# Kernel tuning notes

Measured on AMD Instinct MI355X. Metric: run time of the kernel, lower is better.

## Reference

```python
import jax, jax.numpy as jnp
import numpy as np

N = 100000   # nodes
E = 1600000  # edges (avg degree 16)
D = 128      # input = hidden = out dim
L = 4        # num_layers
EPS = 1e-5   # LayerNorm eps


def setup_inputs() -> dict:
    key = jax.random.key(0)
    k0, k1, k2, k3, k4 = jax.random.split(key, 5)
    in_feat = jax.random.normal(k0, (N, D), dtype=jnp.float32)
    edge_index = jax.random.randint(k1, (2, E), 0, N, dtype=jnp.int32)
    s = 1.0 / np.sqrt(D)
    # GraphConv params per layer: lin_rel (weight+bias), lin_root (weight, no bias)
    W_rel = jax.random.uniform(k2, (L, D, D), jnp.float32, -s, s)
    b_rel = jax.random.uniform(k3, (L, D), jnp.float32, -s, s)
    W_root = jax.random.uniform(k4, (L, D, D), jnp.float32, -s, s)
    # single shared LayerNorm module in the torch code
    ln_gamma = jnp.ones((D,), jnp.float32)
    ln_beta = jnp.zeros((D,), jnp.float32)
    return {"in_feat": in_feat, "edge_index": edge_index, "W_rel": W_rel,
            "b_rel": b_rel, "W_root": W_root, "ln_gamma": ln_gamma, "ln_beta": ln_beta}


def _layer_norm(h, gamma, beta):
    mu = jnp.mean(h, axis=-1, keepdims=True)
    var = jnp.mean(jnp.square(h - mu), axis=-1, keepdims=True)
    return (h - mu) * jax.lax.rsqrt(var + EPS) * gamma + beta


def _graph_conv(h, W_r, b_r, W_rt, src, dst):
    # PyG GraphConv: out_i = lin_rel(sum_{j->i} x_j) + lin_root(x_i)
    agg = jax.ops.segment_sum(h[src], dst, num_segments=N)  # [N, D]
    return agg @ W_r + b_r + h @ W_rt


def reference(in_feat, edge_index, W_rel, b_rel, W_root, ln_gamma, ln_beta):
    src, dst = edge_index[0], edge_index[1]
    # input layer: conv -> ReLU -> LayerNorm -> dropout(p=0)
    h = _graph_conv(in_feat, W_rel[0], b_rel[0], W_root[0], src, dst)
    h = _layer_norm(jax.nn.relu(h), ln_gamma, ln_beta)
    # middle layers with residual
    for l in range(1, L - 1):
        nh = _graph_conv(h, W_rel[l], b_rel[l], W_root[l], src, dst)
        h = _layer_norm(jax.nn.relu(nh + h), ln_gamma, ln_beta)
    # output layer: conv only
    return _graph_conv(h, W_rel[L - 1], b_rel[L - 1], W_root[L - 1], src, dst)
```

## Files before the change

kernel.cpp:

```cpp
#include <hip/hip_runtime.h>
#include <cstddef>

#define N_NODES 100000
#define N_PAD   100032
#define N_EDGES 1600000
#define DIM 128
#define LN_EPS 1e-5f
#define ZROW   N_NODES
#define COL_CAP 3200000

#define B_SHIFT 9
#define B_SIZE  512
#define N_BKT   196
#define EPB     4096
#define NBLK    ((N_EDGES + EPB - 1) / EPB)

typedef short bf16x8 __attribute__((ext_vector_type(8)));
typedef float f32x4 __attribute__((ext_vector_type(4)));
typedef float f32x2 __attribute__((ext_vector_type(2)));

__device__ __forceinline__ float asf(uint u) {
    union { uint i; float f; } c; c.i = u; return c.f;
}
__device__ __forceinline__ float bf2f(uint u) { return asf(u << 16); }
__device__ __forceinline__ ushort f2bf(float x) {
    union { float f; uint i; } c; c.f = x;
    uint r = c.i + 0x7fffu + ((c.i >> 16) & 1u);
    return (ushort)(r >> 16);
}

__device__ __forceinline__ void accp(f32x2* acc, uint p) {
    f32x2 v;
    v.x = asf(p << 16);
    v.y = asf(p & 0xffff0000u);
    *acc += v;
}
__device__ __forceinline__ void accq(f32x2* a, uint4 p) {
    accp(&a[0], p.x); accp(&a[1], p.y); accp(&a[2], p.z); accp(&a[3], p.w);
}


__global__ __launch_bounds__(256) void bhist_kernel(const int* __restrict__ dst,
                                                    int* __restrict__ bcount) {
    __shared__ int lh[N_BKT];
    const int tid = threadIdx.x;
    if (tid < N_BKT) lh[tid] = 0;
    __syncthreads();
    const int base = blockIdx.x * EPB;
    #pragma unroll
    for (int k = 0; k < 16; ++k) {
        int t = base + tid + k * 256;
        if (t < N_EDGES) atomicAdd(&lh[dst[t] >> B_SHIFT], 1);
    }
    __syncthreads();
    if (tid < N_BKT && lh[tid]) atomicAdd(&bcount[tid], lh[tid]);
}

__global__ __launch_bounds__(256) void bscan_kernel(const int* __restrict__ bcount,
                                                    int* __restrict__ bstart,
                                                    int* __restrict__ gcur) {
    __shared__ int s[256];
    const int tid = threadIdx.x;
    int v = (tid < N_BKT) ? bcount[tid] : 0;
    s[tid] = v;
    __syncthreads();
    for (int off = 1; off < 256; off <<= 1) {
        int t = (tid >= off) ? s[tid - off] : 0;
        __syncthreads();
        s[tid] += t;
        __syncthreads();
    }
    if (tid < N_BKT) { int e = s[tid] - v; bstart[tid] = e; gcur[tid] = e; }
    if (tid == 0) bstart[N_BKT] = N_EDGES;
}

__global__ __launch_bounds__(256) void bscatter_kernel(const int* __restrict__ src,
                                                       const int* __restrict__ dst,
                                                       int* __restrict__ gcur,
                                                       int2* __restrict__ pairs) {
    __shared__ int lcnt[N_BKT];
    __shared__ int lbase[N_BKT];
    const int tid = threadIdx.x;
    if (tid < N_BKT) lcnt[tid] = 0;
    __syncthreads();
    const int base = blockIdx.x * EPB;
    int ls[16], ld[16];
    #pragma unroll
    for (int k = 0; k < 16; ++k) {
        int t = base + tid + k * 256;
        if (t < N_EDGES) {
            ls[k] = src[t]; ld[k] = dst[t];
            atomicAdd(&lcnt[ld[k] >> B_SHIFT], 1);
        } else ld[k] = -1;
    }
    __syncthreads();
    if (tid < N_BKT) lbase[tid] = lcnt[tid] ? atomicAdd(&gcur[tid], lcnt[tid]) : 0;
    __syncthreads();
    if (tid < N_BKT) lcnt[tid] = 0;
    __syncthreads();
    #pragma unroll
    for (int k = 0; k < 16; ++k) {
        if (ld[k] >= 0) {
            int b = ld[k] >> B_SHIFT;
            int r = atomicAdd(&lcnt[b], 1);
            pairs[lbase[b] + r] = make_int2(ls[k], ld[k]);
        }
    }
}

__global__ __launch_bounds__(256) void ndeg_kernel(const int2* __restrict__ pairs,
                                                   const int* __restrict__ bstart,
                                                   int* __restrict__ row_ptr,
                                                   int* __restrict__ bpad) {
    __shared__ int ldeg[B_SIZE];
    __shared__ int ws4[4];
    const int b = blockIdx.x;
    const int node0 = b << B_SHIFT;
    const int tid = threadIdx.x;
    ldeg[tid] = 0; ldeg[tid + 256] = 0;
    __syncthreads();
    const int beg = bstart[b], end = bstart[b + 1];
    for (int t = beg + tid; t < end; t += 256)
        atomicAdd(&ldeg[pairs[t].y - node0], 1);
    __syncthreads();
    const int d0 = (ldeg[2 * tid] + 15) & ~15;
    const int d1 = (ldeg[2 * tid + 1] + 15) & ~15;
    const int sum2 = d0 + d1;
    const int lane = tid & 63, wv = tid >> 6;
    int incl = sum2;
    #pragma unroll
    for (int off = 1; off < 64; off <<= 1) {
        int t = __shfl_up(incl, off);
        if (lane >= off) incl += t;
    }
    if (lane == 63) ws4[wv] = incl;
    __syncthreads();
    int woff = 0;
    if (wv > 0) woff += ws4[0];
    if (wv > 1) woff += ws4[1];
    if (wv > 2) woff += ws4[2];
    const int e0 = woff + incl - sum2;
    const int n0 = node0 + 2 * tid;
    if (n0 < N_NODES)     row_ptr[n0]     = e0;
    if (n0 + 1 < N_NODES) row_ptr[n0 + 1] = e0 + d0;
    if (tid == 255) bpad[b] = woff + incl;
}

__global__ __launch_bounds__(256) void pscan_kernel(const int* __restrict__ bpad,
                                                    int* __restrict__ bpadstart) {
    __shared__ int s[256];
    const int tid = threadIdx.x;
    int v = (tid < N_BKT) ? bpad[tid] : 0;
    s[tid] = v;
    __syncthreads();
    for (int off = 1; off < 256; off <<= 1) {
        int t = (tid >= off) ? s[tid - off] : 0;
        __syncthreads();
        s[tid] += t;
        __syncthreads();
    }
    if (tid < N_BKT) bpadstart[tid] = s[tid] - v;
    if (tid == N_BKT - 1) bpadstart[N_BKT] = s[tid];
}

__global__ void addbase_kernel(int* __restrict__ row_ptr, const int* __restrict__ bpadstart) {
    int n = blockIdx.x * 256 + threadIdx.x;
    if (n < N_NODES) row_ptr[n] += bpadstart[n >> B_SHIFT];
    else if (n <= N_PAD) row_ptr[n] = bpadstart[N_BKT];
}

__global__ __launch_bounds__(256) void bfill_kernel(const int2* __restrict__ pairs,
                                                    const int* __restrict__ bstart,
                                                    const int* __restrict__ row_ptr,
                                                    int* __restrict__ col) {
    __shared__ int lcur[B_SIZE];
    const int b = blockIdx.x;
    const int node0 = b << B_SHIFT;
    const int tid = threadIdx.x;
    #pragma unroll
    for (int k = 0; k < 2; ++k) {
        int n = node0 + tid + k * 256;
        lcur[tid + k * 256] = (n < N_NODES) ? row_ptr[n] : 0;
    }
    __syncthreads();
    const int beg = bstart[b], end = bstart[b + 1];
    for (int t = beg + tid; t < end; t += 256) {
        int2 p = pairs[t];
        int r = atomicAdd(&lcur[p.y - node0], 1);
        col[r] = p.x;
    }
    __syncthreads();
    #pragma unroll
    for (int k = 0; k < 2; ++k) {
        int n = tid + k * 256;
        int node = node0 + n;
        if (node < N_NODES) {
            int e = lcur[n];
            int pe = row_ptr[node + 1];
            for (int p = e; p < pe; ++p) col[p] = ZROW;
        }
    }
}


__global__ void cvt_kernel(const float* __restrict__ in, ushort* __restrict__ out) {
    int i = (blockIdx.x * blockDim.x + threadIdx.x) * 4;
    float4 v = *(const float4*)&in[i];
    uint2 r;
    r.x = (uint)f2bf(v.x) | ((uint)f2bf(v.y) << 16);
    r.y = (uint)f2bf(v.z) | ((uint)f2bf(v.w) << 16);
    *(uint2*)&out[i] = r;
}


__global__ void prepack_kernel(const float* __restrict__ Wrel, const float* __restrict__ Wroot,
                               ushort* __restrict__ Wp) {
    int t = blockIdx.x * blockDim.x + threadIdx.x;
    int layer = t >> 12;
    int tl = t & 4095;
    int frag = tl >> 6;
    int lane = tl & 63;
    int ks = frag >> 3, n = frag & 7;
    int c = n * 16 + (lane & 15);
    int k0 = ks * 32 + (lane >> 4) * 8;
    ushort tmp[8];
    #pragma unroll
    for (int j = 0; j < 8; ++j) {
        int kg = k0 + j;
        float w = (kg < 128) ? Wrel[layer * 16384 + kg * 128 + c]
                             : Wroot[layer * 16384 + (kg - 128) * 128 + c];
        tmp[j] = f2bf(w);
    }
    *(uint4*)&Wp[(size_t)t * 8] = *(const uint4*)tmp;
}


template <int MODE>
__global__ __launch_bounds__(256, 5) void fused_kernel(const ushort* __restrict__ hb,
                                                       const int* __restrict__ row_ptr,
                                                       const int* __restrict__ col,
                                                       const ushort* __restrict__ Wp,
                                                       const float* __restrict__ brel,
                                                       const float* __restrict__ gamma,
                                                       const float* __restrict__ beta,
                                                       ushort* __restrict__ outb,
                                                       float* __restrict__ outf) {
    __shared__ char sX[64 * 512];
    const int tid = threadIdx.x;
    const int row0 = blockIdx.x * 64;
    const int lane = tid & 63;
    const int wv = tid >> 6;
    const int rsel = lane >> 4;
    const int c16 = lane & 15;

    for (int c = tid; c < 1024; c += 256) {
        int r = c >> 4, cb = c & 15;
        uint4 v = *(const uint4*)&hb[(size_t)(row0 + r) * 128 + cb * 8];
        *(uint4*)&sX[r * 512 + ((256 + cb * 16) ^ ((r & 7) << 4))] = v;
    }

    const uint4* h4 = (const uint4*)hb;
    #pragma unroll 1
    for (int t = 0; t < 8; ++t) {
        const int rA = wv * 16 + 2 * t;
        const int rB = rA + 1;
        const int p0 = row_ptr[row0 + rA];
        const int p1 = row_ptr[row0 + rA + 1];
        const int p2 = row_ptr[row0 + rA + 2];
        const int itA = (p1 - p0) >> 4;
        const int itB = (p2 - p1) >> 4;
        int jA = p0 + rsel;
        int jB = p1 + rsel;
        const int iters = max(itA, itB);

        f32x2 a[4], b[4];
        #pragma unroll
        for (int u = 0; u < 4; ++u) { a[u] = (f32x2){0.f, 0.f}; b[u] = (f32x2){0.f, 0.f}; }

        for (int it = 0; it < iters; ++it) {
            int sA0 = ZROW, sA1 = ZROW, sA2 = ZROW, sA3 = ZROW;
            int sB0 = ZROW, sB1 = ZROW, sB2 = ZROW, sB3 = ZROW;
            if (it < itA) {
                sA0 = col[jA]; sA1 = col[jA + 4]; sA2 = col[jA + 8]; sA3 = col[jA + 12];
                jA += 16;
            }
            if (it < itB) {
                sB0 = col[jB]; sB1 = col[jB + 4]; sB2 = col[jB + 8]; sB3 = col[jB + 12];
                jB += 16;
            }
            uint4 pA0 = h4[(size_t)sA0 * 16 + c16];
            uint4 pA1 = h4[(size_t)sA1 * 16 + c16];
            uint4 pA2 = h4[(size_t)sA2 * 16 + c16];
            uint4 pA3 = h4[(size_t)sA3 * 16 + c16];
            uint4 pB0 = h4[(size_t)sB0 * 16 + c16];
            uint4 pB1 = h4[(size_t)sB1 * 16 + c16];
            uint4 pB2 = h4[(size_t)sB2 * 16 + c16];
            uint4 pB3 = h4[(size_t)sB3 * 16 + c16];
            accq(a, pA0); accq(a, pA1); accq(a, pA2); accq(a, pA3);
            accq(b, pB0); accq(b, pB1); accq(b, pB2); accq(b, pB3);
        }

        #pragma unroll
        for (int u = 0; u < 4; ++u) {
            float ax = a[u].x, ay = a[u].y, bx = b[u].x, by = b[u].y;
            ax += __shfl_xor(ax, 16); ay += __shfl_xor(ay, 16);
            bx += __shfl_xor(bx, 16); by += __shfl_xor(by, 16);
            ax += __shfl_xor(ax, 32); ay += __shfl_xor(ay, 32);
            bx += __shfl_xor(bx, 32); by += __shfl_xor(by, 32);
            a[u].x = ax; a[u].y = ay; b[u].x = bx; b[u].y = by;
        }
        if (rsel == 0) {
            uint4 o;
            o.x = (uint)f2bf(a[0].x) | ((uint)f2bf(a[0].y) << 16);
            o.y = (uint)f2bf(a[1].x) | ((uint)f2bf(a[1].y) << 16);
            o.z = (uint)f2bf(a[2].x) | ((uint)f2bf(a[2].y) << 16);
            o.w = (uint)f2bf(a[3].x) | ((uint)f2bf(a[3].y) << 16);
            *(uint4*)&sX[rA * 512 + ((c16 * 16) ^ ((rA & 7) << 4))] = o;
        } else if (rsel == 1) {
            uint4 o;
            o.x = (uint)f2bf(b[0].x) | ((uint)f2bf(b[0].y) << 16);
            o.y = (uint)f2bf(b[1].x) | ((uint)f2bf(b[1].y) << 16);
            o.z = (uint)f2bf(b[2].x) | ((uint)f2bf(b[2].y) << 16);
            o.w = (uint)f2bf(b[3].x) | ((uint)f2bf(b[3].y) << 16);
            *(uint4*)&sX[rB * 512 + ((c16 * 16) ^ ((rB & 7) << 4))] = o;
        }
    }
    __syncthreads();

    const int kg = lane >> 4;
    const int cl = lane & 15;
    const int ra = wv * 16 + cl;
    const int abase = ra * 512 + kg * 16;
    const int aswz = (ra & 7) << 4;

    f32x4 acc[8];
    #pragma unroll
    for (int n = 0; n < 8; ++n) acc[n] = (f32x4){0.f, 0.f, 0.f, 0.f};

    const uint4* bp = (const uint4*)Wp + lane;
    #pragma unroll 2
    for (int ks = 0; ks < 8; ++ks) {
        bf16x8 a = *(const bf16x8*)&sX[(abase + ks * 64) ^ aswz];
        #pragma unroll
        for (int n = 0; n < 8; ++n) {
            bf16x8 b = *(const bf16x8*)&bp[(ks * 8 + n) * 64];
            acc[n] = __builtin_amdgcn_mfma_f32_16x16x32_bf16(a, b, acc[n], 0, 0, 0);
        }
    }

    float bias[8], gg[8], bb[8];
    #pragma unroll
    for (int n = 0; n < 8; ++n) {
        int cn = n * 16 + cl;
        bias[n] = brel[cn];
        if (MODE != 2) { gg[n] = gamma[cn]; bb[n] = beta[cn]; }
    }

    #pragma unroll
    for (int reg = 0; reg < 4; ++reg) {
        const int r = wv * 16 + kg * 4 + reg;
        const size_t grow = (size_t)row0 + r;
        const bool live = grow < N_NODES;
        float v[8];
        float s = 0.f, q = 0.f;
        #pragma unroll
        for (int n = 0; n < 8; ++n) {
            float x = acc[n][reg] + bias[n];
            if (MODE == 1) {
                int cn = n * 16 + cl;
                ushort hu = *(const ushort*)&sX[r * 512 + ((256 + 2 * cn) ^ ((r & 7) << 4))];
                x += bf2f(hu);
            }
            if (MODE != 2) x = fmaxf(x, 0.f);
            v[n] = x; s += x; q += x * x;
        }
        if (MODE != 2) {
            #pragma unroll
            for (int m = 8; m >= 1; m >>= 1) { s += __shfl_xor(s, m); q += __shfl_xor(q, m); }
            float mu = s * (1.f / DIM);
            float var = q * (1.f / DIM) - mu * mu;
            float rinv = rsqrtf(var + LN_EPS);
            if (live) {
                #pragma unroll
                for (int n = 0; n < 8; ++n) {
                    float y = (v[n] - mu) * rinv * gg[n] + bb[n];
                    outb[grow * DIM + n * 16 + cl] = f2bf(y);
                }
            }
        } else {
            if (live) {
                #pragma unroll
                for (int n = 0; n < 8; ++n) outf[grow * DIM + n * 16 + cl] = v[n];
            }
        }
    }
}


static inline size_t align256(size_t x) { return (x + 255) & ~(size_t)255; }

extern "C" void kernel_launch(void* const* d_in, const int* in_sizes, int n_in,
                              void* d_out, int out_size, void* d_ws, size_t ws_size,
                              hipStream_t stream) {
    const float* in_feat = (const float*)d_in[0];
    const int*   ei      = (const int*)d_in[1];
    const float* Wrel    = (const float*)d_in[2];
    const float* brel    = (const float*)d_in[3];
    const float* Wroot   = (const float*)d_in[4];
    const float* gamma   = (const float*)d_in[5];
    const float* beta    = (const float*)d_in[6];
    float* out = (float*)d_out;

    char* ws = (char*)d_ws;
    size_t off = 0;
    int* col = (int*)(ws + off);        off = align256(off + (size_t)COL_CAP * 4);
    int2* pairs = (int2*)(ws + off);    off = align256(off + (size_t)N_EDGES * 8);
    int* row_ptr = (int*)(ws + off);    off = align256(off + (size_t)(N_PAD + 2) * 4);
    int* bcount = (int*)(ws + off);     off = align256(off + (size_t)N_BKT * 4);
    int* bstart = (int*)(ws + off);     off = align256(off + (size_t)(N_BKT + 1) * 4);
    int* gcur = (int*)(ws + off);       off = align256(off + (size_t)N_BKT * 4);
    int* bpad = (int*)(ws + off);       off = align256(off + (size_t)N_BKT * 4);
    int* bpadstart = (int*)(ws + off);  off = align256(off + (size_t)(N_BKT + 1) * 4);
    ushort* x0 = (ushort*)(ws + off);   off = align256(off + (size_t)N_PAD * DIM * 2);
    ushort* hA = (ushort*)(ws + off);   off = align256(off + (size_t)N_PAD * DIM * 2);
    ushort* hB = (ushort*)(ws + off);   off = align256(off + (size_t)N_PAD * DIM * 2);
    ushort* Wp = (ushort*)(ws + off);   off = align256(off + (size_t)4 * 256 * 128 * 2);
    (void)ws_size; (void)in_sizes; (void)n_in; (void)out_size;

    const int* src = ei;
    const int* dst = ei + N_EDGES;

    hipMemsetAsync(bcount, 0, (size_t)N_BKT * 4, stream);
    bhist_kernel<<<NBLK, 256, 0, stream>>>(dst, bcount);
    bscan_kernel<<<1, 256, 0, stream>>>(bcount, bstart, gcur);
    bscatter_kernel<<<NBLK, 256, 0, stream>>>(src, dst, gcur, pairs);
    ndeg_kernel<<<N_BKT, 256, 0, stream>>>(pairs, bstart, row_ptr, bpad);
    pscan_kernel<<<1, 256, 0, stream>>>(bpad, bpadstart);
    addbase_kernel<<<(N_PAD + 1 + 255) / 256, 256, 0, stream>>>(row_ptr, bpadstart);
    bfill_kernel<<<N_BKT, 256, 0, stream>>>(pairs, bstart, row_ptr, col);

    const size_t padoff = (size_t)N_NODES * DIM * 2;
    const size_t padlen = (size_t)(N_PAD - N_NODES) * DIM * 2;
    hipMemsetAsync((char*)x0 + padoff, 0, padlen, stream);
    hipMemsetAsync((char*)hA + padoff, 0, padlen, stream);
    hipMemsetAsync((char*)hB + padoff, 0, padlen, stream);

    cvt_kernel<<<(N_NODES * DIM) / (4 * 256), 256, 0, stream>>>(in_feat, x0);
    prepack_kernel<<<64, 256, 0, stream>>>(Wrel, Wroot, Wp);

    const int grid = N_PAD / 64;

    fused_kernel<0><<<grid, 256, 0, stream>>>(x0, row_ptr, col, Wp, brel, gamma, beta, hA, nullptr);
    fused_kernel<1><<<grid, 256, 0, stream>>>(hA, row_ptr, col, Wp + 32768, brel + DIM, gamma, beta, hB, nullptr);
    fused_kernel<1><<<grid, 256, 0, stream>>>(hB, row_ptr, col, Wp + 2 * 32768, brel + 2 * DIM, gamma, beta, hA, nullptr);
    fused_kernel<2><<<grid, 256, 0, stream>>>(hA, row_ptr, col, Wp + 3 * 32768, brel + 3 * DIM, gamma, beta, nullptr, out);
}
```

Before: 425.4 us.

## Halve rows per block and split GEMM columns across waves with shared LayerNorm stats

Each block now covers 32 rows instead of 64, halving shared memory, and the launch-bounds occupancy hint rises from 5 to 8 blocks. In the GEMM stage each wave computes 16 rows by 64 columns instead of 16 by 128. The LayerNorm row statistics are therefore reduced across two waves through a small shared buffer and an extra barrier. The aim is more resident blocks and more latency hiding for the gather, at the cost of twice as many blocks and an extra synchronisation.

```diff
diff --git a/kernel.cpp b/kernel.cpp
--- a/kernel.cpp
+++ b/kernel.cpp
@@ -236,7 +236,7 @@
 
 
 template <int MODE>
-__global__ __launch_bounds__(256, 5) void fused_kernel(const ushort* __restrict__ hb,
+__global__ __launch_bounds__(256, 8) void fused_kernel(const ushort* __restrict__ hb,
                                                        const int* __restrict__ row_ptr,
                                                        const int* __restrict__ col,
                                                        const ushort* __restrict__ Wp,
@@ -245,15 +245,16 @@
                                                        const float* __restrict__ beta,
                                                        ushort* __restrict__ outb,
                                                        float* __restrict__ outf) {
-    __shared__ char sX[64 * 512];
-    const int tid = threadIdx.x;
-    const int row0 = blockIdx.x * 64;
+    __shared__ char sX[32 * 512];
+    __shared__ float2 lnbuf[32][2];
+    const int tid = threadIdx.x;
+    const int row0 = blockIdx.x * 32;
     const int lane = tid & 63;
     const int wv = tid >> 6;
     const int rsel = lane >> 4;
     const int c16 = lane & 15;
 
-    for (int c = tid; c < 1024; c += 256) {
+    for (int c = tid; c < 512; c += 256) {
         int r = c >> 4, cb = c & 15;
         uint4 v = *(const uint4*)&hb[(size_t)(row0 + r) * 128 + cb * 8];
         *(uint4*)&sX[r * 512 + ((256 + cb * 16) ^ ((r & 7) << 4))] = v;
@@ -261,8 +262,8 @@
 
     const uint4* h4 = (const uint4*)hb;
     #pragma unroll 1
-    for (int t = 0; t < 8; ++t) {
-        const int rA = wv * 16 + 2 * t;
+    for (int t = 0; t < 4; ++t) {
+        const int rA = wv * 8 + 2 * t;
         const int rB = rA + 1;
         const int p0 = row_ptr[row0 + rA];
         const int p1 = row_ptr[row0 + rA + 1];
@@ -329,68 +330,97 @@
 
     const int kg = lane >> 4;
     const int cl = lane & 15;
-    const int ra = wv * 16 + cl;
+    const int r0 = (wv & 1) * 16;
+    const int ch = wv >> 1;
+    const int ra = r0 + cl;
     const int abase = ra * 512 + kg * 16;
     const int aswz = (ra & 7) << 4;
 
-    f32x4 acc[8];
-    #pragma unroll
-    for (int n = 0; n < 8; ++n) acc[n] = (f32x4){0.f, 0.f, 0.f, 0.f};
+    f32x4 acc[4];
+    #pragma unroll
+    for (int n = 0; n < 4; ++n) acc[n] = (f32x4){0.f, 0.f, 0.f, 0.f};
 
     const uint4* bp = (const uint4*)Wp + lane;
-    #pragma unroll 2
+    #pragma unroll
     for (int ks = 0; ks < 8; ++ks) {
         bf16x8 a = *(const bf16x8*)&sX[(abase + ks * 64) ^ aswz];
         #pragma unroll
-        for (int n = 0; n < 8; ++n) {
-            bf16x8 b = *(const bf16x8*)&bp[(ks * 8 + n) * 64];
+        for (int n = 0; n < 4; ++n) {
+            bf16x8 b = *(const bf16x8*)&bp[(ks * 8 + ch * 4 + n) * 64];
             acc[n] = __builtin_amdgcn_mfma_f32_16x16x32_bf16(a, b, acc[n], 0, 0, 0);
         }
     }
 
-    float bias[8], gg[8], bb[8];
-    #pragma unroll
-    for (int n = 0; n < 8; ++n) {
-        int cn = n * 16 + cl;
+    float bias[4], gg[4], bb[4];
+    #pragma unroll
+    for (int n = 0; n < 4; ++n) {
+        int cn = ch * 64 + n * 16 + cl;
         bias[n] = brel[cn];
         if (MODE != 2) { gg[n] = gamma[cn]; bb[n] = beta[cn]; }
     }
 
+    float vv[4][4];
+    float ss[4], qq[4];
     #pragma unroll
     for (int reg = 0; reg < 4; ++reg) {
-        const int r = wv * 16 + kg * 4 + reg;
-        const size_t grow = (size_t)row0 + r;
-        const bool live = grow < N_NODES;
-        float v[8];
+        const int r = r0 + kg * 4 + reg;
         float s = 0.f, q = 0.f;
         #pragma unroll
-        for (int n = 0; n < 8; ++n) {
+        for (int n = 0; n < 4; ++n) {
             float x = acc[n][reg] + bias[n];
             if (MODE == 1) {
-                int cn = n * 16 + cl;
+                int cn = ch * 64 + n * 16 + cl;
                 ushort hu = *(const ushort*)&sX[r * 512 + ((256 + 2 * cn) ^ ((r & 7) << 4))];
                 x += bf2f(hu);
             }
             if (MODE != 2) x = fmaxf(x, 0.f);
-            v[n] = x; s += x; q += x * x;
-        }
-        if (MODE != 2) {
+            vv[reg][n] = x; s += x; q += x * x;
+        }
+        ss[reg] = s; qq[reg] = q;
+    }
+
+    if (MODE != 2) {
+        #pragma unroll
+        for (int reg = 0; reg < 4; ++reg) {
             #pragma unroll
-            for (int m = 8; m >= 1; m >>= 1) { s += __shfl_xor(s, m); q += __shfl_xor(q, m); }
+            for (int m = 8; m >= 1; m >>= 1) {
+                ss[reg] += __shfl_xor(ss[reg], m);
+                qq[reg] += __shfl_xor(qq[reg], m);
+            }
+        }
+        if (cl == 0) {
+            #pragma unroll
+            for (int reg = 0; reg < 4; ++reg)
+                lnbuf[r0 + kg * 4 + reg][ch] = make_float2(ss[reg], qq[reg]);
+        }
+        __syncthreads();
+        #pragma unroll
+        for (int reg = 0; reg < 4; ++reg) {
+            const int r = r0 + kg * 4 + reg;
+            const size_t grow = (size_t)row0 + r;
+            float2 e0 = lnbuf[r][0], e1 = lnbuf[r][1];
+            float s = e0.x + e1.x;
+            float q = e0.y + e1.y;
             float mu = s * (1.f / DIM);
             float var = q * (1.f / DIM) - mu * mu;
             float rinv = rsqrtf(var + LN_EPS);
-            if (live) {
+            if (grow < N_NODES) {
                 #pragma unroll
-                for (int n = 0; n < 8; ++n) {
-                    float y = (v[n] - mu) * rinv * gg[n] + bb[n];
-                    outb[grow * DIM + n * 16 + cl] = f2bf(y);
+                for (int n = 0; n < 4; ++n) {
+                    float y = (vv[reg][n] - mu) * rinv * gg[n] + bb[n];
+                    outb[grow * DIM + ch * 64 + n * 16 + cl] = f2bf(y);
                 }
             }
-        } else {
-            if (live) {
+        }
+    } else {
+        #pragma unroll
+        for (int reg = 0; reg < 4; ++reg) {
+            const int r = r0 + kg * 4 + reg;
+            const size_t grow = (size_t)row0 + r;
+            if (grow < N_NODES) {
                 #pragma unroll
-                for (int n = 0; n < 8; ++n) outf[grow * DIM + n * 16 + cl] = v[n];
+                for (int n = 0; n < 4; ++n)
+                    outf[grow * DIM + ch * 64 + n * 16 + cl] = vv[reg][n];
             }
         }
     }
@@ -448,7 +478,7 @@
     cvt_kernel<<<(N_NODES * DIM) / (4 * 256), 256, 0, stream>>>(in_feat, x0);
     prepack_kernel<<<64, 256, 0, stream>>>(Wrel, Wroot, Wp);
 
-    const int grid = N_PAD / 64;
+    const int grid = N_PAD / 32;
 
     fused_kernel<0><<<grid, 256, 0, stream>>>(x0, row_ptr, col, Wp, brel, gamma, beta, hA, nullptr);
     fused_kernel<1><<<grid, 256, 0, stream>>>(hA, row_ptr, col, Wp + 32768, brel + DIM, gamma, beta, hB, nullptr);
```

After: 438.2 us. 1.03x slower.

## Fold residual into root weight identity and halve shared memory staging

Applied to the files above, without the earlier changes.

Adds the identity matrix to the lin_root weights for the middle layers, so the residual h is absorbed into the h@W_root GEMM and the separate residual add disappears. The root-half A operand is read directly from global memory instead of being staged in LDS, which halves shared memory per block, and launch bounds rise from 5 to 6 blocks per CU. The risk is that uncoalesced global reads of A fragments inside the MFMA loop add latency, and folding the residual into bf16 weights (1+w) loses precision on the residual path.

```diff
diff --git a/kernel.cpp b/kernel.cpp
--- a/kernel.cpp
+++ b/kernel.cpp
@@ -217,18 +217,23 @@
                                ushort* __restrict__ Wp) {
     int t = blockIdx.x * blockDim.x + threadIdx.x;
     int layer = t >> 12;
-    int tl = t & 4095;
-    int frag = tl >> 6;
-    int lane = tl & 63;
+    int m = (t >> 11) & 1;
+    int frag = (t >> 6) & 31;
+    int lane = t & 63;
     int ks = frag >> 3, n = frag & 7;
     int c = n * 16 + (lane & 15);
     int k0 = ks * 32 + (lane >> 4) * 8;
     ushort tmp[8];
     #pragma unroll
     for (int j = 0; j < 8; ++j) {
-        int kg = k0 + j;
-        float w = (kg < 128) ? Wrel[layer * 16384 + kg * 128 + c]
-                             : Wroot[layer * 16384 + (kg - 128) * 128 + c];
+        int k = k0 + j;
+        float w;
+        if (m == 0) {
+            w = Wrel[layer * 16384 + k * 128 + c];
+        } else {
+            w = Wroot[layer * 16384 + k * 128 + c];
+            if ((layer == 1 || layer == 2) && k == c) w += 1.0f;
+        }
         tmp[j] = f2bf(w);
     }
     *(uint4*)&Wp[(size_t)t * 8] = *(const uint4*)tmp;
@@ -236,7 +241,7 @@
 
 
 template <int MODE>
-__global__ __launch_bounds__(256, 5) void fused_kernel(const ushort* __restrict__ hb,
+__global__ __launch_bounds__(256, 6) void fused_kernel(const ushort* __restrict__ hb,
                                                        const int* __restrict__ row_ptr,
                                                        const int* __restrict__ col,
                                                        const ushort* __restrict__ Wp,
@@ -245,19 +250,13 @@
                                                        const float* __restrict__ beta,
                                                        ushort* __restrict__ outb,
                                                        float* __restrict__ outf) {
-    __shared__ char sX[64 * 512];
+    __shared__ char sA[64 * 256];
     const int tid = threadIdx.x;
     const int row0 = blockIdx.x * 64;
     const int lane = tid & 63;
     const int wv = tid >> 6;
     const int rsel = lane >> 4;
     const int c16 = lane & 15;
-
-    for (int c = tid; c < 1024; c += 256) {
-        int r = c >> 4, cb = c & 15;
-        uint4 v = *(const uint4*)&hb[(size_t)(row0 + r) * 128 + cb * 8];
-        *(uint4*)&sX[r * 512 + ((256 + cb * 16) ^ ((r & 7) << 4))] = v;
-    }
 
     const uint4* h4 = (const uint4*)hb;
     #pragma unroll 1
@@ -315,14 +314,14 @@
             o.y = (uint)f2bf(a[1].x) | ((uint)f2bf(a[1].y) << 16);
             o.z = (uint)f2bf(a[2].x) | ((uint)f2bf(a[2].y) << 16);
             o.w = (uint)f2bf(a[3].x) | ((uint)f2bf(a[3].y) << 16);
-            *(uint4*)&sX[rA * 512 + ((c16 * 16) ^ ((rA & 7) << 4))] = o;
+            *(uint4*)&sA[rA * 256 + ((c16 * 16) ^ ((rA & 7) << 4))] = o;
         } else if (rsel == 1) {
             uint4 o;
             o.x = (uint)f2bf(b[0].x) | ((uint)f2bf(b[0].y) << 16);
             o.y = (uint)f2bf(b[1].x) | ((uint)f2bf(b[1].y) << 16);
             o.z = (uint)f2bf(b[2].x) | ((uint)f2bf(b[2].y) << 16);
             o.w = (uint)f2bf(b[3].x) | ((uint)f2bf(b[3].y) << 16);
-            *(uint4*)&sX[rB * 512 + ((c16 * 16) ^ ((rB & 7) << 4))] = o;
+            *(uint4*)&sA[rB * 256 + ((c16 * 16) ^ ((rB & 7) << 4))] = o;
         }
     }
     __syncthreads();
@@ -330,20 +329,31 @@
     const int kg = lane >> 4;
     const int cl = lane & 15;
     const int ra = wv * 16 + cl;
-    const int abase = ra * 512 + kg * 16;
+    const size_t growa = (size_t)row0 + ra;
+    const int abase = ra * 256 + kg * 16;
     const int aswz = (ra & 7) << 4;
 
     f32x4 acc[8];
     #pragma unroll
     for (int n = 0; n < 8; ++n) acc[n] = (f32x4){0.f, 0.f, 0.f, 0.f};
 
-    const uint4* bp = (const uint4*)Wp + lane;
-    #pragma unroll 2
-    for (int ks = 0; ks < 8; ++ks) {
-        bf16x8 a = *(const bf16x8*)&sX[(abase + ks * 64) ^ aswz];
+    const uint4* bR = (const uint4*)Wp + lane;
+    const uint4* bT = (const uint4*)(Wp + 16384) + lane;
+    #pragma unroll
+    for (int ks = 0; ks < 4; ++ks) {
+        bf16x8 a = *(const bf16x8*)&sA[(abase + ks * 64) ^ aswz];
         #pragma unroll
         for (int n = 0; n < 8; ++n) {
-            bf16x8 b = *(const bf16x8*)&bp[(ks * 8 + n) * 64];
+            bf16x8 b = *(const bf16x8*)&bR[(ks * 8 + n) * 64];
+            acc[n] = __builtin_amdgcn_mfma_f32_16x16x32_bf16(a, b, acc[n], 0, 0, 0);
+        }
+    }
+    #pragma unroll
+    for (int ks = 0; ks < 4; ++ks) {
+        bf16x8 a = *(const bf16x8*)&hb[growa * 128 + ks * 32 + kg * 8];
+        #pragma unroll
+        for (int n = 0; n < 8; ++n) {
+            bf16x8 b = *(const bf16x8*)&bT[(ks * 8 + n) * 64];
             acc[n] = __builtin_amdgcn_mfma_f32_16x16x32_bf16(a, b, acc[n], 0, 0, 0);
         }
     }
@@ -366,11 +376,6 @@
         #pragma unroll
         for (int n = 0; n < 8; ++n) {
             float x = acc[n][reg] + bias[n];
-            if (MODE == 1) {
-                int cn = n * 16 + cl;
-                ushort hu = *(const ushort*)&sX[r * 512 + ((256 + 2 * cn) ^ ((r & 7) << 4))];
-                x += bf2f(hu);
-            }
             if (MODE != 2) x = fmaxf(x, 0.f);
             v[n] = x; s += x; q += x * x;
         }
@@ -424,7 +429,7 @@
     ushort* x0 = (ushort*)(ws + off);   off = align256(off + (size_t)N_PAD * DIM * 2);
     ushort* hA = (ushort*)(ws + off);   off = align256(off + (size_t)N_PAD * DIM * 2);
     ushort* hB = (ushort*)(ws + off);   off = align256(off + (size_t)N_PAD * DIM * 2);
-    ushort* Wp = (ushort*)(ws + off);   off = align256(off + (size_t)4 * 256 * 128 * 2);
+    ushort* Wp = (ushort*)(ws + off);   off = align256(off + (size_t)4 * 2 * 128 * 128 * 2);
     (void)ws_size; (void)in_sizes; (void)n_in; (void)out_size;
 
     const int* src = ei;
@@ -451,7 +456,7 @@
     const int grid = N_PAD / 64;
 
     fused_kernel<0><<<grid, 256, 0, stream>>>(x0, row_ptr, col, Wp, brel, gamma, beta, hA, nullptr);
-    fused_kernel<1><<<grid, 256, 0, stream>>>(hA, row_ptr, col, Wp + 32768, brel + DIM, gamma, beta, hB, nullptr);
-    fused_kernel<1><<<grid, 256, 0, stream>>>(hB, row_ptr, col, Wp + 2 * 32768, brel + 2 * DIM, gamma, beta, hA, nullptr);
+    fused_kernel<0><<<grid, 256, 0, stream>>>(hA, row_ptr, col, Wp + 32768, brel + DIM, gamma, beta, hB, nullptr);
+    fused_kernel<0><<<grid, 256, 0, stream>>>(hB, row_ptr, col, Wp + 2 * 32768, brel + 2 * DIM, gamma, beta, hA, nullptr);
     fused_kernel<2><<<grid, 256, 0, stream>>>(hA, row_ptr, col, Wp + 3 * 32768, brel + 3 * DIM, gamma, beta, nullptr, out);
 }
```

New measurement: 449.2 us. 5.6% more time.
